# Kernel tuning notes

Measured on AMD Instinct MI355X. Metric: run time of the kernel, lower is better.

Reference implementation:

```python
import jax, jax.numpy as jnp
import numpy as np

# ---- static configuration (matches init_kwargs) ----
N_QUBITS = 11
N_LAYERS = 2
N_HIDDEN = N_QUBITS // 2            # 5
N_VISIBLE = N_QUBITS - N_HIDDEN     # 6
N_PARAMS = N_LAYERS * (3 * N_HIDDEN + (N_HIDDEN - 1) + 3 * N_VISIBLE)  # 74
TWO_PI = 2.0 * np.pi

# Pauli building blocks (numpy constants, complex64)
I2 = np.eye(2, dtype=np.complex64)
X2 = np.array([[0, 1], [1, 0]], dtype=np.complex64)
K2 = np.array([[0, -1], [1, 0]], dtype=np.complex64)   # -i*Y
Z2 = np.array([[1, 0], [0, -1]], dtype=np.complex64)

# PauliZ sign table: wire 0 is the most-significant bit of the flattened state
_idx = np.arange(2 ** N_QUBITS)
SIGNS = np.stack([1.0 - 2.0 * ((_idx >> (N_QUBITS - 1 - q)) & 1)
                  for q in range(N_QUBITS)], 0).astype(np.float32)  # [n_qubits, 2^n]


def _rx(t):
    t = jnp.asarray(t, jnp.float32)
    c, s = jnp.cos(t / 2), jnp.sin(t / 2)
    return (c[..., None, None] * I2 - 1j * s[..., None, None] * X2).astype(jnp.complex64)


def _ry(t):
    t = jnp.asarray(t, jnp.float32)
    c, s = jnp.cos(t / 2), jnp.sin(t / 2)
    return (c[..., None, None] * I2 + s[..., None, None] * K2).astype(jnp.complex64)


def _rz(t):
    t = jnp.asarray(t, jnp.float32)
    c, s = jnp.cos(t / 2), jnp.sin(t / 2)
    return (c[..., None, None] * I2 - 1j * s[..., None, None] * Z2).astype(jnp.complex64)


def _apply_1q(state, gate, q):
    # state: (B,) + (2,)*N_QUBITS ; gate: [2,2] shared or [B,2,2] batched
    s = jnp.moveaxis(state, 1 + q, -1)
    if gate.ndim == 3:
        s = jnp.einsum('bij,b...j->b...i', gate, s)
    else:
        s = jnp.einsum('ij,...j->...i', gate, s)
    return jnp.moveaxis(s, -1, 1 + q)


def _apply_crx(state, theta, c, t):
    # controlled-RX(theta) with control wire c, target wire t (theta scalar)
    sc = jnp.moveaxis(state, [1 + c, 1 + t], [1, 2])
    g = _rx(theta)  # [2,2]
    s1 = jnp.einsum('ij,bj...->bi...', g, sc[:, 1])
    sc = jnp.stack([sc[:, 0], s1], axis=1)
    return jnp.moveaxis(sc, [1, 2], [1 + c, 1 + t])


def _embed_state(angles):
    # Angle embedding: RX(angle_q)|0> on each wire -> product state
    B = angles.shape[0]
    amp = _rx(angles)[..., :, 0]          # [B, n_qubits, 2] (first column = action on |0>)
    st = amp[:, 0]                        # [B, 2]
    for q in range(1, N_QUBITS):
        st = (st[:, :, None] * amp[:, q][:, None, :]).reshape(B, -1)
    return st.reshape((B,) + (2,) * N_QUBITS)


def _circuit(angles, params):
    st = _embed_state(angles)
    p = 0
    for _ in range(N_LAYERS):
        for i in range(N_HIDDEN):
            st = _apply_1q(st, _rx(params[p]), i)
            st = _apply_1q(st, _ry(params[p + 1]), i)
            st = _apply_1q(st, _rz(params[p + 2]), i)
            p += 3
        for i in range(N_HIDDEN - 1):
            st = _apply_crx(st, params[p], i, i + 1)
            p += 1
        for i in range(N_VISIBLE):
            w = N_HIDDEN + i
            st = _apply_1q(st, _rx(params[p]), w)
            st = _apply_1q(st, _ry(params[p + 1]), w)
            st = _apply_1q(st, _rz(params[p + 2]), w)
            p += 3
    probs = (st.real ** 2 + st.imag ** 2).reshape(st.shape[0], -1)  # [B, 2^n]
    return jnp.einsum('bi,qi->bq', probs, SIGNS)  # <Z_q> per qubit, [B, n_qubits]


def _preprocess(x_t):
    # mean-pool feature vector down to n_visible, then min-max scale to [0, 2pi]
    F = x_t.shape[-1]
    step = F // N_VISIBLE
    starts = np.arange(N_VISIBLE) * step
    win = x_t[:, starts[:, None] + np.arange(step)]   # [B, n_visible, step]
    pooled = win.mean(-1)
    mn = pooled.min(-1, keepdims=True)
    mx = pooled.max(-1, keepdims=True)
    return TWO_PI * (pooled - mn) / (mx - mn + 1e-8)


def setup_inputs() -> dict:
    key = jax.random.key(0)
    k1, k2 = jax.random.split(key)
    x = jax.random.normal(k1, (128, 48, 60), dtype=jnp.float32)
    hidden = jnp.zeros((128, N_HIDDEN), dtype=jnp.float32)
    params = jax.random.uniform(k2, (N_PARAMS,), dtype=jnp.float32,
                                minval=0.0, maxval=TWO_PI)
    return {"x": x, "hidden": hidden, "params": params}


def reference(x, hidden, params):
    def body(h, x_t):
        inp = _preprocess(x_t)                         # [B, n_visible]
        angles = jnp.concatenate([h, inp], axis=-1)    # [B, n_qubits]
        z = _circuit(angles, params)                   # [B, n_qubits]
        return z[:, :N_HIDDEN], z[:, N_HIDDEN:]

    xs = jnp.swapaxes(x, 0, 1)                         # [S, B, F]
    hidden_final, outs = jax.lax.scan(body, hidden, xs)
    outputs = jnp.swapaxes(outs, 0, 1)                 # [B, S, n_visible]
    return outputs, hidden_final
```

## Files before the change

### kernel.cpp

```cpp
#include <hip/hip_runtime.h>
#include <math.h>

#define TSTEPS 48
#define FEAT 60
#define BATCH 128
#define BLOCK 256
#define TWO_PI_F 6.2831853071795864769f


struct Cf { float r, i; };
__device__ __forceinline__ Cf cmul(Cf a, Cf b){ return {a.r*b.r - a.i*b.i, a.r*b.i + a.i*b.r}; }
__device__ __forceinline__ Cf cadd(Cf a, Cf b){ return {a.r+b.r, a.i+b.i}; }
__device__ __forceinline__ void mm2(const Cf A[4], const Cf B[4], Cf D[4]) {
  D[0] = cadd(cmul(A[0],B[0]), cmul(A[1],B[2]));
  D[1] = cadd(cmul(A[0],B[1]), cmul(A[1],B[3]));
  D[2] = cadd(cmul(A[2],B[0]), cmul(A[3],B[2]));
  D[3] = cadd(cmul(A[2],B[1]), cmul(A[3],B[3]));
}

__device__ __forceinline__ void fusedU(const float* p, Cf U[4]) {
  float cx = __cosf(0.5f*p[0]), sxn = __sinf(0.5f*p[0]);
  float cy = __cosf(0.5f*p[1]), syn = __sinf(0.5f*p[1]);
  float cz = __cosf(0.5f*p[2]), szn = __sinf(0.5f*p[2]);
  Cf RX[4] = {{cx,0.f},{0.f,-sxn},{0.f,-sxn},{cx,0.f}};
  Cf RY[4] = {{cy,0.f},{-syn,0.f},{syn,0.f},{cy,0.f}};
  Cf RZ[4] = {{cz,-szn},{0.f,0.f},{0.f,0.f},{cz,szn}};
  Cf M[4];
  mm2(RY, RX, M);
  mm2(RZ, M, U);
}

template<int CTRL>
__device__ __forceinline__ float dppf(float v) {
  return __int_as_float(__builtin_amdgcn_mov_dpp(__float_as_int(v), CTRL, 0xF, 0xF, true));
}

template<int M>
__device__ __forceinline__ float sx(float v) {
  if constexpr (M == 1)      return dppf<0xB1>(v);
  else if constexpr (M == 2) return dppf<0x4E>(v);
  else if constexpr (M == 3) return dppf<0x1B>(v);
  else if constexpr (M == 4) return dppf<0x141>(dppf<0x1B>(v));
  else                       return dppf<0x128>(v);
}

template<int M>
__device__ __forceinline__ Cf sxc(Cf v){ return { sx<M>(v.r), sx<M>(v.i) }; }

__device__ __forceinline__ float wave_sum(float v) {
  v += dppf<0x121>(v);
  v += dppf<0x122>(v);
  v += dppf<0x124>(v);
  v += dppf<0x128>(v);
  v += dppf<0x142>(v);
  v += dppf<0x143>(v);
  return __int_as_float(__builtin_amdgcn_readlane(__float_as_int(v), 63));
}

typedef float v2f __attribute__((ext_vector_type(2)));
__device__ __forceinline__ v2f pk_fma(v2f a, v2f b, v2f c) {
  v2f d;
  asm("v_pk_fma_f32 %0, %1, %2, %3" : "=v"(d) : "v"(a), "v"(b), "v"(c));
  return d;
}
__device__ __forceinline__ v2f pk_mul(v2f a, v2f b) {
  v2f d;
  asm("v_pk_mul_f32 %0, %1, %2" : "=v"(d) : "v"(a), "v"(b));
  return d;
}

__device__ __forceinline__ float2 conjmul(float2 a, float2 b) {
  return make_float2(a.x*b.x + a.y*b.y, a.x*b.y - a.y*b.x);
}

template<int M>
__device__ __forceinline__ void lane_u(Cf A[4], const Cf U[4], int hi) {
  Cf ca = hi ? U[3] : U[0];
  Cf cb = hi ? U[2] : U[1];
  #pragma unroll
  for (int r = 0; r < 4; ++r) {
    Cf o = sxc<M>(A[r]);
    A[r] = cadd(cmul(ca, A[r]), cmul(cb, o));
  }
}
template<int M>
__device__ __forceinline__ void lane_crx(Cf A[4], float c, float s, int cv) {
  float cc = cv ? c : 1.f, ss = cv ? s : 0.f;
  #pragma unroll
  for (int r = 0; r < 4; ++r) {
    Cf o = sxc<M>(A[r]);
    A[r] = { cc*A[r].r + ss*o.i, cc*A[r].i - ss*o.r };
  }
}
__device__ __forceinline__ void reg_u_b1(Cf A[4], const Cf U[4]) {
  #pragma unroll
  for (int k = 0; k < 2; ++k) {
    Cf a0 = A[k], a1 = A[k+2];
    A[k]   = cadd(cmul(U[0], a0), cmul(U[1], a1));
    A[k+2] = cadd(cmul(U[2], a0), cmul(U[3], a1));
  }
}
__device__ __forceinline__ void reg_u_b0(Cf A[4], const Cf U[4]) {
  #pragma unroll
  for (int k = 0; k < 4; k += 2) {
    Cf a0 = A[k], a1 = A[k+1];
    A[k]   = cadd(cmul(U[0], a0), cmul(U[1], a1));
    A[k+1] = cadd(cmul(U[2], a0), cmul(U[3], a1));
  }
}
__device__ __forceinline__ void reg_crx_b1(Cf A[4], float c, float s, int cv) {
  float cc = cv ? c : 1.f, ss = cv ? s : 0.f;
  #pragma unroll
  for (int k = 0; k < 2; ++k) {
    Cf a0 = A[k], a1 = A[k+2];
    A[k]   = { cc*a0.r + ss*a1.i, cc*a0.i - ss*a1.r };
    A[k+2] = { ss*a0.i + cc*a1.r, -ss*a0.r + cc*a1.i };
  }
}
__device__ __forceinline__ void reg_crx_b0c1(Cf A[4], float c, float s) {
  Cf a0 = A[2], a1 = A[3];
  A[2] = { c*a0.r + s*a1.i, c*a0.i - s*a1.r };
  A[3] = { s*a0.i + c*a1.r, -s*a0.r + c*a1.i };
}

template<int NTs, int D>
__device__ __forceinline__ void stageK(const float2* __restrict__ src,
                                       float2* __restrict__ dst,
                                       const float2* __restrict__ Pq, int tid) {
  const int total = 5*3*NTs*D*D;
  for (int tau = tid; tau < total; tau += BLOCK) {
    int K = tau % D;
    int J = (tau / D) % D;
    int rest = tau / (D*D);
    int t = rest % NTs;
    int s = (rest / NTs) % 3;
    int m = rest / (3*NTs);
    const float2* Sb = src + (m*NTs + t)*(4*D*D);
    const float2* Pm = Pq + s*4;
    float ax = 0.f, ay = 0.f;
    #pragma unroll
    for (int a = 0; a < 2; ++a)
      #pragma unroll
      for (int bb = 0; bb < 2; ++bb) {
        float2 g = Sb[(2*J+a)*(2*D) + (2*K+bb)];
        float2 p = Pm[bb*2 + a];
        ax += g.x*p.x - g.y*p.y;
        ay += g.x*p.y + g.y*p.x;
      }
    dst[tau] = make_float2(ax, ay);
  }
}

__global__ __launch_bounds__(BLOCK)
void qrnn_kernel(const float* __restrict__ x, const float* __restrict__ hin,
                 const float* __restrict__ params, float* __restrict__ out) {
  __shared__ __align__(16) char bufA[30720];
  __shared__ __align__(16) char bufB[23040];
  __shared__ float coefL[5*256];
  __shared__ float2 Pl[5*12];
  __shared__ float2 U2l[5*4];
  __shared__ float crxcl[8], crxsl[8];
  __shared__ float Wl[6*8];

  const int b   = blockIdx.x;
  const int tid = threadIdx.x;

  float2* Vp  = (float2*)bufB;
  float4* Vp4 = (float4*)bufB;
  float2* A1  = (float2*)bufA;
  float2* A2  = (float2*)bufB;
  float2* A3  = (float2*)bufA;
  float2* A4  = (float2*)bufB;

  if (tid < 5) {
    int q = tid;
    Cf U1[4]; fusedU(params + 3*q, U1);
    Cf T[4] = {U1[0], {-U1[1].r,-U1[1].i}, U1[2], {-U1[3].r,-U1[3].i}};
    Cf Ud[4] = {{U1[0].r,-U1[0].i},{U1[2].r,-U1[2].i},
                {U1[1].r,-U1[1].i},{U1[3].r,-U1[3].i}};
    Cf Zt[4]; mm2(T, Ud, Zt);
    Cf Ty[4] = {{-U1[1].i, U1[1].r}, {U1[0].i, -U1[0].r},
                {-U1[3].i, U1[3].r}, {U1[2].i, -U1[2].r}};
    Cf Yt[4]; mm2(Ty, Ud, Yt);
    float2* P = Pl + q*12;
    P[0] = make_float2(1.f,0.f); P[1] = make_float2(0.f,0.f);
    P[2] = make_float2(0.f,0.f); P[3] = make_float2(1.f,0.f);
    #pragma unroll
    for (int e = 0; e < 4; ++e) P[4+e] = make_float2(Zt[e].r, Zt[e].i);
    #pragma unroll
    for (int e = 0; e < 4; ++e) P[8+e] = make_float2(-Yt[e].r, -Yt[e].i);
  } else if (tid >= 64 && tid < 69) {
    int q = tid - 64;
    Cf U2[4]; fusedU(params + 37 + 3*q, U2);
    #pragma unroll
    for (int e = 0; e < 4; ++e) U2l[q*4+e] = make_float2(U2[e].r, U2[e].i);
  } else if (tid >= 128 && tid < 136) {
    int i = tid - 128;
    float th = (i < 4) ? params[15 + i] : params[52 + (i - 4)];
    crxcl[i] = __cosf(0.5f*th); crxsl[i] = __sinf(0.5f*th);
  } else if (tid >= 192 && tid < 198) {
    int k = tid - 192;
    Cf Ua[4], Ub[4], W[4];
    fusedU(params + 19 + 3*k, Ua);
    fusedU(params + 56 + 3*k, Ub);
    mm2(Ub, Ua, W);
    #pragma unroll
    for (int e = 0; e < 4; ++e) { Wl[k*8+2*e] = W[e].r; Wl[k*8+2*e+1] = W[e].i; }
  }
  __syncthreads();

  {
    const int quad = tid & 7, col = tid >> 3;
    const int vb2 = quad & 1, vb3 = (quad >> 1) & 1, vb4 = quad >> 2;
    Cf A[4];
    #pragma unroll
    for (int r = 0; r < 4; ++r)
      A[r] = { ((quad<<2)|r) == col ? 1.f : 0.f, 0.f };
    Cf U2g[5][4];
    #pragma unroll
    for (int q = 0; q < 5; ++q)
      #pragma unroll
      for (int e = 0; e < 4; ++e)
        U2g[q][e] = { U2l[q*4+e].x, U2l[q*4+e].y };
    float c_[8], s_[8];
    #pragma unroll
    for (int g = 0; g < 8; ++g) { c_[g] = crxcl[g]; s_[g] = crxsl[g]; }
    lane_crx<2>(A, c_[0], s_[0], vb4);
    lane_crx<1>(A, c_[1], s_[1], vb3);
    reg_crx_b1 (A, c_[2], s_[2], vb2);
    reg_crx_b0c1(A, c_[3], s_[3]);
    lane_u<4>(A, U2g[0], vb4);
    lane_u<2>(A, U2g[1], vb3);
    lane_u<1>(A, U2g[2], vb2);
    reg_u_b1 (A, U2g[3]);
    reg_u_b0 (A, U2g[4]);
    lane_crx<2>(A, c_[4], s_[4], vb4);
    lane_crx<1>(A, c_[5], s_[5], vb3);
    reg_crx_b1 (A, c_[6], s_[6], vb2);
    reg_crx_b0c1(A, c_[7], s_[7]);
    #pragma unroll
    for (int r = 0; r < 4; ++r)
      Vp[((quad<<2)|r)*32 + col] = make_float2(A[r].r, A[r].i);
  }
  __syncthreads();

  {
    const int jt = tid >> 4, kt = tid & 15;
    float2 T[2][2], Bm[5][2][2];
    #pragma unroll
    for (int a = 0; a < 2; ++a)
      #pragma unroll
      for (int c2 = 0; c2 < 2; ++c2) {
        T[a][c2] = make_float2(0.f, 0.f);
        #pragma unroll
        for (int m = 0; m < 5; ++m) Bm[m][a][c2] = make_float2(0.f, 0.f);
      }
    #pragma unroll
    for (int i = 0; i < 32; ++i) {
      float4 vj = Vp4[i*16 + jt], vk = Vp4[i*16 + kt];
      float2 vj0{vj.x,vj.y}, vj1{vj.z,vj.w}, vk0{vk.x,vk.y}, vk1{vk.z,vk.w};
      float2 p[2][2] = {{conjmul(vj0,vk0), conjmul(vj0,vk1)},
                        {conjmul(vj1,vk0), conjmul(vj1,vk1)}};
      #pragma unroll
      for (int a = 0; a < 2; ++a)
        #pragma unroll
        for (int c2 = 0; c2 < 2; ++c2) {
          T[a][c2].x += p[a][c2].x; T[a][c2].y += p[a][c2].y;
        }
      #pragma unroll
      for (int m = 0; m < 5; ++m)
        if (i & (16 >> m)) {
          #pragma unroll
          for (int a = 0; a < 2; ++a)
            #pragma unroll
            for (int c2 = 0; c2 < 2; ++c2) {
              Bm[m][a][c2].x += p[a][c2].x; Bm[m][a][c2].y += p[a][c2].y;
            }
        }
    }
    float2 P4[12];
    #pragma unroll
    for (int e = 0; e < 12; ++e) P4[e] = Pl[4*12 + e];
    #pragma unroll
    for (int m = 0; m < 5; ++m) {
      float2 G[2][2];
      #pragma unroll
      for (int a = 0; a < 2; ++a)
        #pragma unroll
        for (int c2 = 0; c2 < 2; ++c2)
          G[a][c2] = make_float2(T[a][c2].x - 2.f*Bm[m][a][c2].x,
                                 T[a][c2].y - 2.f*Bm[m][a][c2].y);
      #pragma unroll
      for (int s = 0; s < 3; ++s) {
        float ax = 0.f, ay = 0.f;
        #pragma unroll
        for (int a = 0; a < 2; ++a)
          #pragma unroll
          for (int bb = 0; bb < 2; ++bb) {
            float2 g = G[a][bb];
            float2 p = P4[s*4 + bb*2 + a];
            ax += g.x*p.x - g.y*p.y;
            ay += g.x*p.y + g.y*p.x;
          }
        A1[(m*3 + s)*256 + (jt<<4) + kt] = make_float2(ax, ay);
      }
    }
  }
  __syncthreads();

  stageK<3, 8>(A1, A2, Pl + 3*12, tid);  __syncthreads();
  stageK<9, 4>(A2, A3, Pl + 2*12, tid);  __syncthreads();
  stageK<27,2>(A3, A4, Pl + 1*12, tid);  __syncthreads();
  for (int tau = tid; tau < 5*256; tau += BLOCK) {
    int n = tau & 255, m = tau >> 8;
    float val = 0.f;
    if (n < 243) {
      int t = n % 81, s = n / 81;
      const float2* Sb = A4 + (m*81 + t)*4;
      const float2* Pm = Pl + s*4;
      float ax = 0.f;
      #pragma unroll
      for (int a = 0; a < 2; ++a)
        #pragma unroll
        for (int bb = 0; bb < 2; ++bb) {
          float2 g = Sb[a*2 + bb];
          float2 p = Pm[bb*2 + a];
          ax += g.x*p.x - g.y*p.y;
        }
      val = ax * (1.f/32.f);
    }
    coefL[tau] = val;
  }
  __syncthreads();

  const int w = tid >> 6, lane = tid & 63;
  if (w == 0) {
    v2f sAp[2][5], sBp[2][5], sCp[2][5], cfp[5][2];
    #pragma unroll
    for (int s = 0; s < 2; ++s) {
      #pragma unroll
      for (int half = 0; half < 2; ++half) {
        int n = (2*s + half)*64 + lane;
        int nn = (n < 243) ? n : 0;
        int d0 = nn/81; int rm = nn - d0*81;
        int d1 = rm/27; rm -= d1*27;
        int d2 = rm/9;  rm -= d2*9;
        int d3 = rm/3;  int d4 = rm - d3*3;
        int dq[5] = {d0, d1, d2, d3, d4};
        #pragma unroll
        for (int q = 0; q < 5; ++q) {
          if (half == 0) {
            sAp[s][q].x = (dq[q] == 0) ? 1.f : 0.f;
            sBp[s][q].x = (dq[q] == 1) ? 1.f : 0.f;
            sCp[s][q].x = (dq[q] == 2) ? 1.f : 0.f;
          } else {
            sAp[s][q].y = (dq[q] == 0) ? 1.f : 0.f;
            sBp[s][q].y = (dq[q] == 1) ? 1.f : 0.f;
            sCp[s][q].y = (dq[q] == 2) ? 1.f : 0.f;
          }
        }
      }
    }
    #pragma unroll
    for (int m = 0; m < 5; ++m) {
      cfp[m][0].x = coefL[m*256 + lane];
      cfp[m][0].y = coefL[m*256 + lane + 64];
      cfp[m][1].x = coefL[m*256 + lane + 128];
      cfp[m][1].y = coefL[m*256 + lane + 192];
    }
    const float* hp = hin + b*5;
    float h0 = hp[0], h1 = hp[1], h2 = hp[2], h3 = hp[3], h4 = hp[4];
    #pragma unroll 1
    for (int t = 0; t < TSTEPS; ++t) {
      float cq[5] = {__cosf(h0), __cosf(h1), __cosf(h2), __cosf(h3), __cosf(h4)};
      float sq[5] = {__sinf(h0), __sinf(h1), __sinf(h2), __sinf(h3), __sinf(h4)};
      v2f cqp[5], sqp[5];
      #pragma unroll
      for (int q = 0; q < 5; ++q) {
        cqp[q] = (v2f){cq[q], cq[q]};
        sqp[q] = (v2f){sq[q], sq[q]};
      }
      v2f monoP[2];
      #pragma unroll
      for (int s = 0; s < 2; ++s) {
        v2f f0 = pk_fma(sBp[s][0], cqp[0], pk_fma(sCp[s][0], sqp[0], sAp[s][0]));
        v2f f1 = pk_fma(sBp[s][1], cqp[1], pk_fma(sCp[s][1], sqp[1], sAp[s][1]));
        v2f f2 = pk_fma(sBp[s][2], cqp[2], pk_fma(sCp[s][2], sqp[2], sAp[s][2]));
        v2f f3 = pk_fma(sBp[s][3], cqp[3], pk_fma(sCp[s][3], sqp[3], sAp[s][3]));
        v2f f4 = pk_fma(sBp[s][4], cqp[4], pk_fma(sCp[s][4], sqp[4], sAp[s][4]));
        monoP[s] = pk_mul(pk_mul(pk_mul(f0, f1), pk_mul(f2, f3)), f4);
      }
      float hn[5];
      #pragma unroll
      for (int m = 0; m < 5; ++m) {
        v2f tacc = pk_mul(monoP[0], cfp[m][0]);
        tacc = pk_fma(monoP[1], cfp[m][1], tacc);
        hn[m] = wave_sum(tacc.x + tacc.y);
      }
      h0 = hn[0]; h1 = hn[1]; h2 = hn[2]; h3 = hn[3]; h4 = hn[4];
    }
    if (lane < 5) {
      float hv = (lane==0) ? h0 : (lane==1) ? h1 : (lane==2) ? h2
               : (lane==3) ? h3 : h4;
      out[BATCH*TSTEPS*6 + b*5 + lane] = hv;
    }
  } else if (w == 1 && lane < TSTEPS) {
    const float* xp = x + (size_t)b*(TSTEPS*FEAT) + lane*FEAT;
    const float4* xp4 = (const float4*)xp;
    float4 vv[15];
    #pragma unroll
    for (int i2 = 0; i2 < 15; ++i2) vv[i2] = xp4[i2];
    float el[60];
    #pragma unroll
    for (int i2 = 0; i2 < 15; ++i2) {
      el[4*i2+0] = vv[i2].x; el[4*i2+1] = vv[i2].y;
      el[4*i2+2] = vv[i2].z; el[4*i2+3] = vv[i2].w;
    }
    float pooled[6];
    #pragma unroll
    for (int k = 0; k < 6; ++k) {
      float s = 0.f;
      #pragma unroll
      for (int f = 0; f < 10; ++f) s += el[k*10 + f];
      pooled[k] = s * 0.1f;
    }
    float mn = pooled[0], mx = pooled[0];
    #pragma unroll
    for (int v2 = 1; v2 < 6; ++v2) {
      mn = fminf(mn, pooled[v2]); mx = fmaxf(mx, pooled[v2]);
    }
    float* op = out + (size_t)b*(TSTEPS*6) + lane*6;
    #pragma unroll
    for (int k = 0; k < 6; ++k) {
      float W0r = Wl[k*8+0], W0i = Wl[k*8+1], W1r = Wl[k*8+2], W1i = Wl[k*8+3];
      float W2r = Wl[k*8+4], W2i = Wl[k*8+5], W3r = Wl[k*8+6], W3i = Wl[k*8+7];
      float ang = TWO_PI_F * (pooled[k] - mn) / (mx - mn + 1e-8f);
      float ch = __cosf(0.5f*ang), sh = __sinf(0.5f*ang);
      float v0r = W0r*ch + W1i*sh, v0i = W0i*ch - W1r*sh;
      float v1r = W2r*ch + W3i*sh, v1i = W2i*ch - W3r*sh;
      op[k] = (v0r*v0r + v0i*v0i) - (v1r*v1r + v1i*v1i);
    }
  }
}

extern "C" void kernel_launch(void* const* d_in, const int* in_sizes, int n_in,
                              void* d_out, int out_size, void* d_ws, size_t ws_size,
                              hipStream_t stream) {
  const float* x      = (const float*)d_in[0];
  const float* hidden = (const float*)d_in[1];
  const float* params = (const float*)d_in[2];
  float* out          = (float*)d_out;
  qrnn_kernel<<<dim3(BATCH), dim3(BLOCK), 0, stream>>>(x, hidden, params, out);
}
```

Measured before the change: 83.67 us.

## Double block size to split Gram accumulation and use raw hardware sin/cos

Grows the block to 512 threads and splits the 32-row Gram/accumulation stage into two halves of 16 rows, with one half writing partial results to shared memory and the other adding its own after a barrier. The bit-sign trick for the top qubit is replaced by a per-half sign. The recurrent loop now keeps hidden values pre-scaled by 1/(2π) and calls the native amdgcn sin/cos builtins, skipping the range reduction in __sinf/__cosf. The coefficient scale and final output are adjusted to match. This shortens the serial precompute and each timestep's trig cost, at the price of an extra barrier, more idle threads in the other stages and possible occupancy effects.

```diff
diff --git a/kernel.cpp b/kernel.cpp
--- a/kernel.cpp
+++ b/kernel.cpp
@@ -4,8 +4,9 @@
 #define TSTEPS 48
 #define FEAT 60
 #define BATCH 128
-#define BLOCK 256
+#define BLOCK 512
 #define TWO_PI_F 6.2831853071795864769f
+#define INV2PI_F 0.15915494309189535f
 
 
 struct Cf { float r, i; };
@@ -209,7 +210,7 @@
   }
   __syncthreads();
 
-  {
+  if (tid < 256) {
     const int quad = tid & 7, col = tid >> 3;
     const int vb2 = quad & 1, vb3 = (quad >> 1) & 1, vb4 = quad >> 2;
     Cf A[4];
@@ -245,18 +246,22 @@
   __syncthreads();
 
   {
-    const int jt = tid >> 4, kt = tid & 15;
-    float2 T[2][2], Bm[5][2][2];
+    const int jk = tid & 255;
+    const int jt = jk >> 4, kt = jk & 15;
+    const int half = tid >> 8;
+    const int ibase = half << 4;
+    float2 Tacc[2][2], Bacc[4][2][2];
     #pragma unroll
     for (int a = 0; a < 2; ++a)
       #pragma unroll
       for (int c2 = 0; c2 < 2; ++c2) {
-        T[a][c2] = make_float2(0.f, 0.f);
-        #pragma unroll
-        for (int m = 0; m < 5; ++m) Bm[m][a][c2] = make_float2(0.f, 0.f);
-      }
-    #pragma unroll
-    for (int i = 0; i < 32; ++i) {
+        Tacc[a][c2] = make_float2(0.f, 0.f);
+        #pragma unroll
+        for (int mb = 0; mb < 4; ++mb) Bacc[mb][a][c2] = make_float2(0.f, 0.f);
+      }
+    #pragma unroll
+    for (int ii = 0; ii < 16; ++ii) {
+      const int i = ibase + ii;
       float4 vj = Vp4[i*16 + jt], vk = Vp4[i*16 + kt];
       float2 vj0{vj.x,vj.y}, vj1{vj.z,vj.w}, vk0{vk.x,vk.y}, vk1{vk.z,vk.w};
       float2 p[2][2] = {{conjmul(vj0,vk0), conjmul(vj0,vk1)},
@@ -265,31 +270,38 @@
       for (int a = 0; a < 2; ++a)
         #pragma unroll
         for (int c2 = 0; c2 < 2; ++c2) {
-          T[a][c2].x += p[a][c2].x; T[a][c2].y += p[a][c2].y;
+          Tacc[a][c2].x += p[a][c2].x; Tacc[a][c2].y += p[a][c2].y;
         }
       #pragma unroll
-      for (int m = 0; m < 5; ++m)
-        if (i & (16 >> m)) {
+      for (int mb = 0; mb < 4; ++mb)
+        if (ii & (8 >> mb)) {
           #pragma unroll
           for (int a = 0; a < 2; ++a)
             #pragma unroll
             for (int c2 = 0; c2 < 2; ++c2) {
-              Bm[m][a][c2].x += p[a][c2].x; Bm[m][a][c2].y += p[a][c2].y;
+              Bacc[mb][a][c2].x += p[a][c2].x; Bacc[mb][a][c2].y += p[a][c2].y;
             }
         }
     }
     float2 P4[12];
     #pragma unroll
     for (int e = 0; e < 12; ++e) P4[e] = Pl[4*12 + e];
+    const float sgn0 = half ? -1.f : 1.f;
+    float2 acc[15];
     #pragma unroll
     for (int m = 0; m < 5; ++m) {
       float2 G[2][2];
       #pragma unroll
       for (int a = 0; a < 2; ++a)
         #pragma unroll
-        for (int c2 = 0; c2 < 2; ++c2)
-          G[a][c2] = make_float2(T[a][c2].x - 2.f*Bm[m][a][c2].x,
-                                 T[a][c2].y - 2.f*Bm[m][a][c2].y);
+        for (int c2 = 0; c2 < 2; ++c2) {
+          float2 t = Tacc[a][c2];
+          if (m == 0) G[a][c2] = make_float2(sgn0*t.x, sgn0*t.y);
+          else {
+            float2 bv = Bacc[m-1][a][c2];
+            G[a][c2] = make_float2(t.x - 2.f*bv.x, t.y - 2.f*bv.y);
+          }
+        }
       #pragma unroll
       for (int s = 0; s < 3; ++s) {
         float ax = 0.f, ay = 0.f;
@@ -302,7 +314,19 @@
             ax += g.x*p.x - g.y*p.y;
             ay += g.x*p.y + g.y*p.x;
           }
-        A1[(m*3 + s)*256 + (jt<<4) + kt] = make_float2(ax, ay);
+        acc[m*3 + s] = make_float2(ax, ay);
+      }
+    }
+    if (half) {
+      #pragma unroll
+      for (int e = 0; e < 15; ++e) A1[e*256 + jk] = acc[e];
+    }
+    __syncthreads();
+    if (!half) {
+      #pragma unroll
+      for (int e = 0; e < 15; ++e) {
+        float2 v = A1[e*256 + jk];
+        A1[e*256 + jk] = make_float2(v.x + acc[e].x, v.y + acc[e].y);
       }
     }
   }
@@ -327,7 +351,7 @@
           float2 p = Pm[bb*2 + a];
           ax += g.x*p.x - g.y*p.y;
         }
-      val = ax * (1.f/32.f);
+      val = ax * 4.97359197e-3f;
     }
     coefL[tau] = val;
   }
@@ -369,11 +393,16 @@
       cfp[m][1].y = coefL[m*256 + lane + 192];
     }
     const float* hp = hin + b*5;
-    float h0 = hp[0], h1 = hp[1], h2 = hp[2], h3 = hp[3], h4 = hp[4];
+    float h0 = hp[0]*INV2PI_F, h1 = hp[1]*INV2PI_F, h2 = hp[2]*INV2PI_F,
+          h3 = hp[3]*INV2PI_F, h4 = hp[4]*INV2PI_F;
     #pragma unroll 1
     for (int t = 0; t < TSTEPS; ++t) {
-      float cq[5] = {__cosf(h0), __cosf(h1), __cosf(h2), __cosf(h3), __cosf(h4)};
-      float sq[5] = {__sinf(h0), __sinf(h1), __sinf(h2), __sinf(h3), __sinf(h4)};
+      float cq[5] = {__builtin_amdgcn_cosf(h0), __builtin_amdgcn_cosf(h1),
+                     __builtin_amdgcn_cosf(h2), __builtin_amdgcn_cosf(h3),
+                     __builtin_amdgcn_cosf(h4)};
+      float sq[5] = {__builtin_amdgcn_sinf(h0), __builtin_amdgcn_sinf(h1),
+                     __builtin_amdgcn_sinf(h2), __builtin_amdgcn_sinf(h3),
+                     __builtin_amdgcn_sinf(h4)};
       v2f cqp[5], sqp[5];
       #pragma unroll
       for (int q = 0; q < 5; ++q) {
@@ -402,7 +431,7 @@
     if (lane < 5) {
       float hv = (lane==0) ? h0 : (lane==1) ? h1 : (lane==2) ? h2
                : (lane==3) ? h3 : h4;
-      out[BATCH*TSTEPS*6 + b*5 + lane] = hv;
+      out[BATCH*TSTEPS*6 + b*5 + lane] = TWO_PI_F*hv;
     }
   } else if (w == 1 && lane < TSTEPS) {
     const float* xp = x + (size_t)b*(TSTEPS*FEAT) + lane*FEAT;
```

Result: no change. 82.43 us (-1.5%).
